# Kernel optimization log

Measured on AMD Instinct MI355X. Metric: run time of the kernel, lower is better.

Reference implementation:

```python
import jax, jax.numpy as jnp
import numpy as np

N_TOTAL = 60000   # real + ghost particles (positions/features rows)
N_REAL = 54000    # query/output particles
N_GHOST = N_TOTAL - N_REAL
N_EDGES = 1_000_000
FEAT = 32
SIZE = 3          # RBF basis functions per spatial dim -> 9 tensor-product basis


def setup_inputs() -> dict:
    key = jax.random.key(0)
    ks = jax.random.split(key, 9)
    positions = jax.random.uniform(ks[0], (N_TOTAL, 2), dtype=jnp.float32)
    output = jax.random.uniform(ks[1], (N_REAL, 2), dtype=jnp.float32)
    features = jax.random.normal(ks[2], (N_TOTAL, FEAT), dtype=jnp.float32)
    # real nodes first (-1), then ghosts pointing at a real node index
    ghostIndices = jnp.concatenate([
        jnp.full((N_REAL,), -1, dtype=jnp.int32),
        jax.random.randint(ks[3], (N_GHOST,), 0, N_REAL, dtype=jnp.int32),
    ])
    row = jax.random.randint(ks[4], (N_EDGES,), 0, N_TOTAL, dtype=jnp.int32)  # source (positions)
    col = jax.random.randint(ks[5], (N_EDGES,), 0, N_REAL, dtype=jnp.int32)   # target (output)
    edge_index = jnp.stack([row, col], axis=0)
    support = jnp.float32(0.1)
    scale = 1.0 / np.sqrt(SIZE * SIZE * FEAT)
    W0 = jax.random.normal(ks[6], (SIZE * SIZE, FEAT, FEAT), dtype=jnp.float32) * scale
    W1 = jax.random.normal(ks[7], (SIZE * SIZE, FEAT, FEAT), dtype=jnp.float32) * scale
    W2 = jax.random.normal(ks[8], (SIZE * SIZE, FEAT, FEAT), dtype=jnp.float32) * scale
    return {"positions": positions, "features": features, "output": output,
            "ghostIndices": ghostIndices, "support": support,
            "edge_index": edge_index, "W0": W0, "W1": W1, "W2": W2}


def _rbf_basis(pseudo, size=SIZE):
    """Gaussian tensor-product RBF basis over 2D pseudo-coords in [-1,1]. -> [E, size*size]"""
    centers = jnp.linspace(-1.0, 1.0, size, dtype=pseudo.dtype)
    gamma = (size - 1) / 2.0  # inverse of center spacing
    phi = jnp.exp(-(gamma * (pseudo[..., None] - centers)) ** 2)  # [E, 2, size]
    u, v = phi[:, 0, :], phi[:, 1, :]
    return (u[:, :, None] * v[:, None, :]).reshape(pseudo.shape[0], size * size)


def reference(positions, features, output, ghostIndices, support, edge_index, W0, W1, W2):
    row, col = edge_index[0], edge_index[1]
    M = output.shape[0]
    # per-edge pseudo coordinates: gather, subtract, normalize, clamp
    pseudo = jnp.clip((output[col] - positions[row]) / support, -1.0, 1.0)  # [E, 2]
    basis = _rbf_basis(pseudo)  # [E, 9]
    ghosts = ghostIndices[M:]   # layout: real nodes first, so these are the != -1 entries
    ans = features
    for W, act in ((W0, True), (W1, True), (W2, False)):
        x_src = ans[row]  # [E, k] gather source features (all nodes incl. ghosts)
        # aggregate basis-weighted features at target nodes, then one dense contraction
        T = jax.ops.segment_sum(basis[:, :, None] * x_src[:, None, :], col,
                                num_segments=M)          # [M, 9, k]
        out = jnp.einsum('mbk,bkl->ml', T, W)            # [M, l]
        if act:
            out = jax.nn.relu(out)
        ghostFeatures = out[ghosts]                      # index_select of ghost mirrors
        ans = jnp.concatenate([out, ghostFeatures], axis=0)  # [N_total, l]
    return ans
```

## Files before the change

kernel.cpp:

```cpp
#include <hip/hip_runtime.h>
#include <hip/hip_fp16.h>
#include <hip/hip_bf16.h>

#define M_REAL   54000
#define N_TOT    60000
#define N_EDGE   1000000

typedef __attribute__((ext_vector_type(8)))  short short8;
typedef __attribute__((ext_vector_type(16))) float f32x16;
typedef __attribute__((ext_vector_type(4)))  unsigned int uint4n;

__global__ void build_kernel(const int* __restrict__ row,
                             const int* __restrict__ col,
                             const int* __restrict__ ghost,
                             const float* __restrict__ positions,
                             const float* __restrict__ outpos,
                             const float* __restrict__ supportp,
                             int* __restrict__ counts,
                             uint4n* __restrict__ bucketData,
                             int maxdeg) {
    int e = blockIdx.x * blockDim.x + threadIdx.x;
    if (e >= N_EDGE) return;
    const int c = col[e];
    const int r = row[e];
    const int rm = (r < M_REAL) ? r : ghost[r];
    const float invs = 1.0f / supportp[0];
    float du = (outpos[2 * c]     - positions[2 * r])     * invs;
    float dv = (outpos[2 * c + 1] - positions[2 * r + 1]) * invs;
    du = fminf(fmaxf(du, -1.0f), 1.0f);
    dv = fminf(fmaxf(dv, -1.0f), 1.0f);
    const float u0 = __expf(-(du + 1.f) * (du + 1.f));
    const float u1 = __expf(-du * du);
    const float u2 = __expf(-(du - 1.f) * (du - 1.f));
    const float v0 = __expf(-(dv + 1.f) * (dv + 1.f));
    const float v1 = __expf(-dv * dv);
    const float v2 = __expf(-(dv - 1.f) * (dv - 1.f));
    __half2 h01 = __floats2half2_rn(u0, u1);
    __half2 h20 = __floats2half2_rn(u2, v0);
    __half2 h12 = __floats2half2_rn(v1, v2);
    uint4n d;
    d.x = (unsigned)r | ((unsigned)rm << 16);
    d.y = *reinterpret_cast<unsigned*>(&h01);
    d.z = *reinterpret_cast<unsigned*>(&h20);
    d.w = *reinterpret_cast<unsigned*>(&h12);
    int p = atomicAdd(&counts[c], 1);
    if (p < maxdeg) bucketData[(size_t)c * maxdeg + p] = d;
}

__global__ void pad_kernel(int* __restrict__ counts,
                           uint4n* __restrict__ bucketData,
                           int maxdeg) {
    int m = blockIdx.x * blockDim.x + threadIdx.x;
    if (m >= M_REAL) return;
    int deg = counts[m];
    if (deg > maxdeg) deg = maxdeg;
    int deg4 = (deg + 3) & ~3;
    uint4n z = {0u, 0u, 0u, 0u};
    for (int p = deg; p < deg4; ++p)
        bucketData[(size_t)m * maxdeg + p] = z;
    counts[m] = deg4;
}

__global__ void wprep_kernel(const float* __restrict__ W0,
                             const float* __restrict__ W1,
                             const float* __restrict__ W2,
                             unsigned short* __restrict__ Wt) {
    int i = blockIdx.x * blockDim.x + threadIdx.x;
    if (i >= 3 * 9216) return;
    const int layer = i / 9216;
    const int rem   = i % 9216;
    const int k     = rem >> 5;
    const int l     = rem & 31;
    const float* src = (layer == 0) ? W0 : (layer == 1 ? W1 : W2);
    __hip_bfloat16 b = __float2bfloat16(src[rem]);
    Wt[layer * 9216 + l * 288 + k] = __builtin_bit_cast(unsigned short, b);
}

__global__ __launch_bounds__(256) void edge_kernel(
        const float* __restrict__ xin,
        const int*   __restrict__ counts,
        const uint4n* __restrict__ bucketData,
        unsigned short* __restrict__ Tb,
        int use_hi, int maxdeg) {
    const int lane = threadIdx.x & 31;
    const int slot = threadIdx.x >> 5;
    const int m = blockIdx.x * 8 + slot;

    float t[9];
#pragma unroll
    for (int b = 0; b < 9; ++b) t[b] = 0.0f;

    const int deg4 = counts[m];
    const uint4n* bd = bucketData + (size_t)m * maxdeg;

    for (int i = 0; i < deg4; i += 4) {
        uint4n q[4];
#pragma unroll
        for (int j = 0; j < 4; ++j) q[j] = bd[i + j];
        float x[4];
#pragma unroll
        for (int j = 0; j < 4; ++j) {
            const unsigned rr = use_hi ? (q[j].x >> 16) : (q[j].x & 0xffffu);
            x[j] = xin[(size_t)rr * 32 + lane];
        }
#pragma unroll
        for (int j = 0; j < 4; ++j) {
            unsigned qy = q[j].y, qz = q[j].z, qw = q[j].w;
            const float2 U01  = __half22float2(*reinterpret_cast<const __half2*>(&qy));
            const float2 U2V0 = __half22float2(*reinterpret_cast<const __half2*>(&qz));
            const float2 V12  = __half22float2(*reinterpret_cast<const __half2*>(&qw));
            const float xv = x[j];
            const float vx0 = U2V0.y * xv;
            const float vx1 = V12.x * xv;
            const float vx2 = V12.y * xv;
            t[0] += U01.x * vx0;  t[1] += U01.x * vx1;  t[2] += U01.x * vx2;
            t[3] += U01.y * vx0;  t[4] += U01.y * vx1;  t[5] += U01.y * vx2;
            t[6] += U2V0.x * vx0; t[7] += U2V0.x * vx1; t[8] += U2V0.x * vx2;
        }
    }

    unsigned short* tr = Tb + (size_t)m * 288 + lane;
#pragma unroll
    for (int b = 0; b < 9; ++b) {
        __hip_bfloat16 h = __float2bfloat16(t[b]);
        tr[b * 32] = __builtin_bit_cast(unsigned short, h);
    }
}

__global__ __launch_bounds__(256, 2) void gemm_kernel(
        const unsigned short* __restrict__ Tb,
        const unsigned short* __restrict__ Wt,
        float* __restrict__ yout,
        int act) {
    const int wave = threadIdx.x >> 6;
    const int lane = threadIdx.x & 63;
    const int col  = lane & 31;
    const int kh   = lane >> 5;
    const int m0   = (blockIdx.x * 4 + wave) * 32;

    const int row  = m0 + col;
    const int rowc = (row < M_REAL) ? row : (M_REAL - 1);
    const uint4n* a = reinterpret_cast<const uint4n*>(Tb + (size_t)rowc * 288) + kh;
    const uint4n* b = reinterpret_cast<const uint4n*>(Wt + (size_t)col * 288) + kh;

    f32x16 acc = {};
#pragma unroll
    for (int s = 0; s < 18; ++s) {
        union { uint4n u; short8 v; } av, bv;
        av.u = a[s * 2];
        bv.u = b[s * 2];
        acc = __builtin_amdgcn_mfma_f32_32x32x16_bf16(av.v, bv.v, acc, 0, 0, 0);
    }

#pragma unroll
    for (int r = 0; r < 16; ++r) {
        const int rr = (r & 3) + 8 * (r >> 2) + 4 * kh;
        const int om = m0 + rr;
        float v = acc[r];
        if (act) v = fmaxf(v, 0.0f);
        if (om < M_REAL) yout[om * 32 + col] = v;
    }
}

__global__ void ghost_kernel(const int* __restrict__ ghost,
                             float* __restrict__ out) {
    int idx = blockIdx.x * blockDim.x + threadIdx.x;
    if (idx >= (N_TOT - M_REAL) * 32) return;
    int i = idx >> 5;
    int k = idx & 31;
    int g = ghost[M_REAL + i];
    out[(M_REAL + i) * 32 + k] = out[g * 32 + k];
}

extern "C" void kernel_launch(void* const* d_in, const int* in_sizes, int n_in,
                              void* d_out, int out_size, void* d_ws, size_t ws_size,
                              hipStream_t stream) {
    const float* positions = (const float*)d_in[0];
    const float* features  = (const float*)d_in[1];
    const float* outpos    = (const float*)d_in[2];
    const int*   ghost     = (const int*)d_in[3];
    const float* support   = (const float*)d_in[4];
    const int*   edge      = (const int*)d_in[5];
    const float* W0        = (const float*)d_in[6];
    const float* W1        = (const float*)d_in[7];
    const float* W2        = (const float*)d_in[8];
    float* out = (float*)d_out;

    auto al = [](size_t x) { return (x + 255) & ~(size_t)255; };
    const size_t countsB = al((size_t)M_REAL * 4);
    const size_t TbB     = al((size_t)M_REAL * 288 * 2);
    const size_t WtB     = al((size_t)3 * 9216 * 2);
    const size_t outB    = al((size_t)M_REAL * 32 * 4);
    const size_t need64  = countsB + (size_t)M_REAL * 64 * 16 + TbB + WtB + outB;
    const int maxdeg = (ws_size >= need64) ? 64 : 48;

    char* ws = (char*)d_ws;
    int*            counts     = (int*)ws;            ws += countsB;
    uint4n*         bucketData = (uint4n*)ws;         ws += (size_t)M_REAL * maxdeg * 16;
    unsigned short* Tb         = (unsigned short*)ws; ws += TbB;
    unsigned short* Wt         = (unsigned short*)ws; ws += WtB;
    float*          out1       = (float*)ws;
    float*          out0       = out;

    const int* erow = edge;
    const int* ecol = edge + N_EDGE;

    (void)hipMemsetAsync(counts, 0, (size_t)M_REAL * 4, stream);
    build_kernel<<<(N_EDGE + 255) / 256, 256, 0, stream>>>(
        erow, ecol, ghost, positions, outpos, support, counts, bucketData, maxdeg);
    pad_kernel<<<(M_REAL + 255) / 256, 256, 0, stream>>>(counts, bucketData, maxdeg);
    wprep_kernel<<<(3 * 9216 + 255) / 256, 256, 0, stream>>>(W0, W1, W2, Wt);

    const int egrid = M_REAL / 8;
    const int ggrid = 422;

    edge_kernel<<<egrid, 256, 0, stream>>>(features, counts, bucketData, Tb, 0, maxdeg);
    gemm_kernel<<<ggrid, 256, 0, stream>>>(Tb, Wt, out0, 1);
    edge_kernel<<<egrid, 256, 0, stream>>>(out0, counts, bucketData, Tb, 1, maxdeg);
    gemm_kernel<<<ggrid, 256, 0, stream>>>(Tb, Wt + 9216, out1, 1);
    edge_kernel<<<egrid, 256, 0, stream>>>(out1, counts, bucketData, Tb, 1, maxdeg);
    gemm_kernel<<<ggrid, 256, 0, stream>>>(Tb, Wt + 2 * 9216, out, 0);

    ghost_kernel<<<((N_TOT - M_REAL) * 32 + 255) / 256, 256, 0, stream>>>(ghost, out);
}
```

Measured before the change: 194.5 us.

## Replace fixed-capacity per-node buckets with compact CSR via count, scan, scatter

Edge binning moves from fixed maxdeg-slot buckets per target node, padded to multiples of 4, to a compact CSR layout built with a count pass, a single-block prefix scan and an atomic-cursor scatter. The edge kernel now reads by offsets and masks tail entries instead of relying on zero padding. This removes the silent truncation of edges above maxdeg, and the compact layout may improve cache locality of the edge stream. In exchange it adds an extra pass over col and a serial single-block scan, and edge reads are no longer 4-aligned per node.

```diff
diff --git a/kernel.cpp b/kernel.cpp
--- a/kernel.cpp
+++ b/kernel.cpp
@@ -10,15 +10,54 @@
 typedef __attribute__((ext_vector_type(16))) float f32x16;
 typedef __attribute__((ext_vector_type(4)))  unsigned int uint4n;
 
-__global__ void build_kernel(const int* __restrict__ row,
-                             const int* __restrict__ col,
-                             const int* __restrict__ ghost,
-                             const float* __restrict__ positions,
-                             const float* __restrict__ outpos,
-                             const float* __restrict__ supportp,
-                             int* __restrict__ counts,
-                             uint4n* __restrict__ bucketData,
-                             int maxdeg) {
+__global__ void count_kernel(const int* __restrict__ col,
+                             int* __restrict__ counts) {
+    int e = blockIdx.x * blockDim.x + threadIdx.x;
+    if (e >= N_EDGE) return;
+    atomicAdd(&counts[col[e]], 1);
+}
+
+__global__ __launch_bounds__(256) void scan_kernel(
+        const int* __restrict__ counts,
+        int* __restrict__ offsets,
+        int* __restrict__ cursor,
+        uint4n* __restrict__ bucketData) {
+    __shared__ int part[256];
+    const int tid = threadIdx.x;
+    const int CH = (M_REAL + 255) / 256;
+    const int lo = tid * CH;
+    const int hi = (lo + CH < M_REAL) ? lo + CH : M_REAL;
+    int s = 0;
+    for (int i = lo; i < hi; ++i) s += counts[i];
+    part[tid] = s;
+    __syncthreads();
+    for (int d = 1; d < 256; d <<= 1) {
+        int t = (tid >= d) ? part[tid - d] : 0;
+        __syncthreads();
+        if (tid >= d) part[tid] += t;
+        __syncthreads();
+    }
+    int run = part[tid] - s;
+    for (int i = lo; i < hi; ++i) {
+        offsets[i] = run;
+        cursor[i]  = run;
+        run += counts[i];
+    }
+    if (tid == 255) offsets[M_REAL] = part[255];
+    if (tid < 4) {
+        uint4n z = {0u, 0u, 0u, 0u};
+        bucketData[N_EDGE + tid] = z;
+    }
+}
+
+__global__ void scatter_kernel(const int* __restrict__ row,
+                               const int* __restrict__ col,
+                               const int* __restrict__ ghost,
+                               const float* __restrict__ positions,
+                               const float* __restrict__ outpos,
+                               const float* __restrict__ supportp,
+                               int* __restrict__ cursor,
+                               uint4n* __restrict__ bucketData) {
     int e = blockIdx.x * blockDim.x + threadIdx.x;
     if (e >= N_EDGE) return;
     const int c = col[e];
@@ -43,22 +82,8 @@
     d.y = *reinterpret_cast<unsigned*>(&h01);
     d.z = *reinterpret_cast<unsigned*>(&h20);
     d.w = *reinterpret_cast<unsigned*>(&h12);
-    int p = atomicAdd(&counts[c], 1);
-    if (p < maxdeg) bucketData[(size_t)c * maxdeg + p] = d;
-}
-
-__global__ void pad_kernel(int* __restrict__ counts,
-                           uint4n* __restrict__ bucketData,
-                           int maxdeg) {
-    int m = blockIdx.x * blockDim.x + threadIdx.x;
-    if (m >= M_REAL) return;
-    int deg = counts[m];
-    if (deg > maxdeg) deg = maxdeg;
-    int deg4 = (deg + 3) & ~3;
-    uint4n z = {0u, 0u, 0u, 0u};
-    for (int p = deg; p < deg4; ++p)
-        bucketData[(size_t)m * maxdeg + p] = z;
-    counts[m] = deg4;
+    int p = atomicAdd(&cursor[c], 1);
+    bucketData[p] = d;
 }
 
 __global__ void wprep_kernel(const float* __restrict__ W0,
@@ -78,10 +103,10 @@
 
 __global__ __launch_bounds__(256) void edge_kernel(
         const float* __restrict__ xin,
-        const int*   __restrict__ counts,
+        const int*   __restrict__ offsets,
         const uint4n* __restrict__ bucketData,
         unsigned short* __restrict__ Tb,
-        int use_hi, int maxdeg) {
+        int use_hi) {
     const int lane = threadIdx.x & 31;
     const int slot = threadIdx.x >> 5;
     const int m = blockIdx.x * 8 + slot;
@@ -90,10 +115,11 @@
 #pragma unroll
     for (int b = 0; b < 9; ++b) t[b] = 0.0f;
 
-    const int deg4 = counts[m];
-    const uint4n* bd = bucketData + (size_t)m * maxdeg;
-
-    for (int i = 0; i < deg4; i += 4) {
+    const int beg = offsets[m];
+    const int deg = offsets[m + 1] - beg;
+    const uint4n* bd = bucketData + beg;
+
+    for (int i = 0; i < deg; i += 4) {
         uint4n q[4];
 #pragma unroll
         for (int j = 0; j < 4; ++j) q[j] = bd[i + j];
@@ -101,7 +127,8 @@
 #pragma unroll
         for (int j = 0; j < 4; ++j) {
             const unsigned rr = use_hi ? (q[j].x >> 16) : (q[j].x & 0xffffu);
-            x[j] = xin[(size_t)rr * 32 + lane];
+            const float xv = xin[(size_t)rr * 32 + lane];
+            x[j] = (i + j < deg) ? xv : 0.0f;
         }
 #pragma unroll
         for (int j = 0; j < 4; ++j) {
@@ -187,18 +214,13 @@
     float* out = (float*)d_out;
 
     auto al = [](size_t x) { return (x + 255) & ~(size_t)255; };
-    const size_t countsB = al((size_t)M_REAL * 4);
-    const size_t TbB     = al((size_t)M_REAL * 288 * 2);
-    const size_t WtB     = al((size_t)3 * 9216 * 2);
-    const size_t outB    = al((size_t)M_REAL * 32 * 4);
-    const size_t need64  = countsB + (size_t)M_REAL * 64 * 16 + TbB + WtB + outB;
-    const int maxdeg = (ws_size >= need64) ? 64 : 48;
-
     char* ws = (char*)d_ws;
-    int*            counts     = (int*)ws;            ws += countsB;
-    uint4n*         bucketData = (uint4n*)ws;         ws += (size_t)M_REAL * maxdeg * 16;
-    unsigned short* Tb         = (unsigned short*)ws; ws += TbB;
-    unsigned short* Wt         = (unsigned short*)ws; ws += WtB;
+    int*            counts     = (int*)ws;            ws += al((size_t)M_REAL * 4);
+    int*            offsets    = (int*)ws;            ws += al((size_t)(M_REAL + 1) * 4);
+    int*            cursor     = (int*)ws;            ws += al((size_t)M_REAL * 4);
+    uint4n*         bucketData = (uint4n*)ws;         ws += al((size_t)(N_EDGE + 4) * 16);
+    unsigned short* Tb         = (unsigned short*)ws; ws += al((size_t)M_REAL * 288 * 2);
+    unsigned short* Wt         = (unsigned short*)ws; ws += al((size_t)3 * 9216 * 2);
     float*          out1       = (float*)ws;
     float*          out0       = out;
 
@@ -206,19 +228,20 @@
     const int* ecol = edge + N_EDGE;
 
     (void)hipMemsetAsync(counts, 0, (size_t)M_REAL * 4, stream);
-    build_kernel<<<(N_EDGE + 255) / 256, 256, 0, stream>>>(
-        erow, ecol, ghost, positions, outpos, support, counts, bucketData, maxdeg);
-    pad_kernel<<<(M_REAL + 255) / 256, 256, 0, stream>>>(counts, bucketData, maxdeg);
+    count_kernel<<<(N_EDGE + 255) / 256, 256, 0, stream>>>(ecol, counts);
+    scan_kernel<<<1, 256, 0, stream>>>(counts, offsets, cursor, bucketData);
+    scatter_kernel<<<(N_EDGE + 255) / 256, 256, 0, stream>>>(
+        erow, ecol, ghost, positions, outpos, support, cursor, bucketData);
     wprep_kernel<<<(3 * 9216 + 255) / 256, 256, 0, stream>>>(W0, W1, W2, Wt);
 
     const int egrid = M_REAL / 8;
     const int ggrid = 422;
 
-    edge_kernel<<<egrid, 256, 0, stream>>>(features, counts, bucketData, Tb, 0, maxdeg);
+    edge_kernel<<<egrid, 256, 0, stream>>>(features, offsets, bucketData, Tb, 0);
     gemm_kernel<<<ggrid, 256, 0, stream>>>(Tb, Wt, out0, 1);
-    edge_kernel<<<egrid, 256, 0, stream>>>(out0, counts, bucketData, Tb, 1, maxdeg);
+    edge_kernel<<<egrid, 256, 0, stream>>>(out0, offsets, bucketData, Tb, 1);
     gemm_kernel<<<ggrid, 256, 0, stream>>>(Tb, Wt + 9216, out1, 1);
-    edge_kernel<<<egrid, 256, 0, stream>>>(out1, counts, bucketData, Tb, 1, maxdeg);
+    edge_kernel<<<egrid, 256, 0, stream>>>(out1, offsets, bucketData, Tb, 1);
     gemm_kernel<<<ggrid, 256, 0, stream>>>(Tb, Wt + 2 * 9216, out, 0);
 
     ghost_kernel<<<((N_TOT - M_REAL) * 32 + 255) / 256, 256, 0, stream>>>(ghost, out);
```

Measured after the change: 351.5 us. 1.81x slower.

## Fuse edge aggregation and MFMA contraction into one per-layer kernel via LDS

Applied to the files above, without the earlier changes.

Merges the per-layer edge aggregation and the bf16 MFMA GEMM into a single kernel. Each block aggregates 32 target nodes into a padded shared-memory tile, then one wave runs the 32x32x288 contraction from LDS. This removes the global round trip of the T buffer and three kernel launches. In exchange, only one wave out of four does the GEMM, each block serialises four nodes per half-wave, and the __syncthreads barrier can leave lanes idle when degrees are uneven.

```diff
diff --git a/kernel.cpp b/kernel.cpp
--- a/kernel.cpp
+++ b/kernel.cpp
@@ -5,6 +5,7 @@
 #define M_REAL   54000
 #define N_TOT    60000
 #define N_EDGE   1000000
+#define TSTRIDE  296
 
 typedef __attribute__((ext_vector_type(8)))  short short8;
 typedef __attribute__((ext_vector_type(16))) float f32x16;
@@ -76,89 +77,87 @@
     Wt[layer * 9216 + l * 288 + k] = __builtin_bit_cast(unsigned short, b);
 }
 
-__global__ __launch_bounds__(256) void edge_kernel(
+__global__ __launch_bounds__(256) void conv_kernel(
         const float* __restrict__ xin,
         const int*   __restrict__ counts,
         const uint4n* __restrict__ bucketData,
-        unsigned short* __restrict__ Tb,
-        int use_hi, int maxdeg) {
-    const int lane = threadIdx.x & 31;
-    const int slot = threadIdx.x >> 5;
-    const int m = blockIdx.x * 8 + slot;
-
-    float t[9];
-#pragma unroll
-    for (int b = 0; b < 9; ++b) t[b] = 0.0f;
-
-    const int deg4 = counts[m];
-    const uint4n* bd = bucketData + (size_t)m * maxdeg;
-
-    for (int i = 0; i < deg4; i += 4) {
-        uint4n q[4];
-#pragma unroll
-        for (int j = 0; j < 4; ++j) q[j] = bd[i + j];
-        float x[4];
-#pragma unroll
-        for (int j = 0; j < 4; ++j) {
-            const unsigned rr = use_hi ? (q[j].x >> 16) : (q[j].x & 0xffffu);
-            x[j] = xin[(size_t)rr * 32 + lane];
-        }
-#pragma unroll
-        for (int j = 0; j < 4; ++j) {
-            unsigned qy = q[j].y, qz = q[j].z, qw = q[j].w;
-            const float2 U01  = __half22float2(*reinterpret_cast<const __half2*>(&qy));
-            const float2 U2V0 = __half22float2(*reinterpret_cast<const __half2*>(&qz));
-            const float2 V12  = __half22float2(*reinterpret_cast<const __half2*>(&qw));
-            const float xv = x[j];
-            const float vx0 = U2V0.y * xv;
-            const float vx1 = V12.x * xv;
-            const float vx2 = V12.y * xv;
-            t[0] += U01.x * vx0;  t[1] += U01.x * vx1;  t[2] += U01.x * vx2;
-            t[3] += U01.y * vx0;  t[4] += U01.y * vx1;  t[5] += U01.y * vx2;
-            t[6] += U2V0.x * vx0; t[7] += U2V0.x * vx1; t[8] += U2V0.x * vx2;
-        }
-    }
-
-    unsigned short* tr = Tb + (size_t)m * 288 + lane;
-#pragma unroll
-    for (int b = 0; b < 9; ++b) {
-        __hip_bfloat16 h = __float2bfloat16(t[b]);
-        tr[b * 32] = __builtin_bit_cast(unsigned short, h);
-    }
-}
-
-__global__ __launch_bounds__(256, 2) void gemm_kernel(
-        const unsigned short* __restrict__ Tb,
         const unsigned short* __restrict__ Wt,
         float* __restrict__ yout,
-        int act) {
-    const int wave = threadIdx.x >> 6;
-    const int lane = threadIdx.x & 63;
-    const int col  = lane & 31;
-    const int kh   = lane >> 5;
-    const int m0   = (blockIdx.x * 4 + wave) * 32;
-
-    const int row  = m0 + col;
-    const int rowc = (row < M_REAL) ? row : (M_REAL - 1);
-    const uint4n* a = reinterpret_cast<const uint4n*>(Tb + (size_t)rowc * 288) + kh;
-    const uint4n* b = reinterpret_cast<const uint4n*>(Wt + (size_t)col * 288) + kh;
-
-    f32x16 acc = {};
-#pragma unroll
-    for (int s = 0; s < 18; ++s) {
-        union { uint4n u; short8 v; } av, bv;
-        av.u = a[s * 2];
-        bv.u = b[s * 2];
-        acc = __builtin_amdgcn_mfma_f32_32x32x16_bf16(av.v, bv.v, acc, 0, 0, 0);
+        int act, int use_hi, int maxdeg) {
+    __shared__ unsigned short Tl[32 * TSTRIDE];
+
+    const int lane = threadIdx.x & 31;
+    const int hw   = threadIdx.x >> 5;
+    const int m0   = blockIdx.x * 32;
+
+    for (int r = 0; r < 4; ++r) {
+        const int dl = hw * 4 + r;
+        const int m  = m0 + dl;
+
+        float t[9];
+#pragma unroll
+        for (int b = 0; b < 9; ++b) t[b] = 0.0f;
+
+        if (m < M_REAL) {
+            const int deg4 = counts[m];
+            const uint4n* bd = bucketData + (size_t)m * maxdeg;
+            for (int i = 0; i < deg4; i += 4) {
+                uint4n q[4];
+#pragma unroll
+                for (int j = 0; j < 4; ++j) q[j] = bd[i + j];
+                float x[4];
+#pragma unroll
+                for (int j = 0; j < 4; ++j) {
+                    const unsigned rr = use_hi ? (q[j].x >> 16) : (q[j].x & 0xffffu);
+                    x[j] = xin[(size_t)rr * 32 + lane];
+                }
+#pragma unroll
+                for (int j = 0; j < 4; ++j) {
+                    unsigned qy = q[j].y, qz = q[j].z, qw = q[j].w;
+                    const float2 U01  = __half22float2(*reinterpret_cast<const __half2*>(&qy));
+                    const float2 U2V0 = __half22float2(*reinterpret_cast<const __half2*>(&qz));
+                    const float2 V12  = __half22float2(*reinterpret_cast<const __half2*>(&qw));
+                    const float xv = x[j];
+                    const float vx0 = U2V0.y * xv;
+                    const float vx1 = V12.x * xv;
+                    const float vx2 = V12.y * xv;
+                    t[0] += U01.x * vx0;  t[1] += U01.x * vx1;  t[2] += U01.x * vx2;
+                    t[3] += U01.y * vx0;  t[4] += U01.y * vx1;  t[5] += U01.y * vx2;
+                    t[6] += U2V0.x * vx0; t[7] += U2V0.x * vx1; t[8] += U2V0.x * vx2;
+                }
+            }
+        }
+        unsigned short* tr = &Tl[dl * TSTRIDE + lane];
+#pragma unroll
+        for (int b = 0; b < 9; ++b) {
+            __hip_bfloat16 h = __float2bfloat16(t[b]);
+            tr[b * 32] = __builtin_bit_cast(unsigned short, h);
+        }
     }
-
-#pragma unroll
-    for (int r = 0; r < 16; ++r) {
-        const int rr = (r & 3) + 8 * (r >> 2) + 4 * kh;
-        const int om = m0 + rr;
-        float v = acc[r];
-        if (act) v = fmaxf(v, 0.0f);
-        if (om < M_REAL) yout[om * 32 + col] = v;
+    __syncthreads();
+
+    if (threadIdx.x < 64) {
+        const int l31 = threadIdx.x & 31;
+        const int kh  = threadIdx.x >> 5;
+        const unsigned short* brow = Wt + (size_t)l31 * 288 + kh * 8;
+
+        f32x16 acc = {};
+#pragma unroll
+        for (int s = 0; s < 18; ++s) {
+            short8 av = *reinterpret_cast<const short8*>(&Tl[l31 * TSTRIDE + s * 16 + kh * 8]);
+            union { uint4n u; short8 v; } bv;
+            bv.u = *reinterpret_cast<const uint4n*>(brow + s * 16);
+            acc = __builtin_amdgcn_mfma_f32_32x32x16_bf16(av, bv.v, acc, 0, 0, 0);
+        }
+
+#pragma unroll
+        for (int r = 0; r < 16; ++r) {
+            const int rr = (r & 3) + 8 * (r >> 2) + 4 * kh;
+            const int om = m0 + rr;
+            float v = acc[r];
+            if (act) v = fmaxf(v, 0.0f);
+            if (om < M_REAL) yout[om * 32 + l31] = v;
+        }
     }
 }
 
@@ -188,16 +187,14 @@
 
     auto al = [](size_t x) { return (x + 255) & ~(size_t)255; };
     const size_t countsB = al((size_t)M_REAL * 4);
-    const size_t TbB     = al((size_t)M_REAL * 288 * 2);
     const size_t WtB     = al((size_t)3 * 9216 * 2);
     const size_t outB    = al((size_t)M_REAL * 32 * 4);
-    const size_t need64  = countsB + (size_t)M_REAL * 64 * 16 + TbB + WtB + outB;
+    const size_t need64  = countsB + (size_t)M_REAL * 64 * 16 + WtB + outB;
     const int maxdeg = (ws_size >= need64) ? 64 : 48;
 
     char* ws = (char*)d_ws;
     int*            counts     = (int*)ws;            ws += countsB;
     uint4n*         bucketData = (uint4n*)ws;         ws += (size_t)M_REAL * maxdeg * 16;
-    unsigned short* Tb         = (unsigned short*)ws; ws += TbB;
     unsigned short* Wt         = (unsigned short*)ws; ws += WtB;
     float*          out1       = (float*)ws;
     float*          out0       = out;
@@ -211,15 +208,14 @@
     pad_kernel<<<(M_REAL + 255) / 256, 256, 0, stream>>>(counts, bucketData, maxdeg);
     wprep_kernel<<<(3 * 9216 + 255) / 256, 256, 0, stream>>>(W0, W1, W2, Wt);
 
-    const int egrid = M_REAL / 8;
-    const int ggrid = 422;
-
-    edge_kernel<<<egrid, 256, 0, stream>>>(features, counts, bucketData, Tb, 0, maxdeg);
-    gemm_kernel<<<ggrid, 256, 0, stream>>>(Tb, Wt, out0, 1);
-    edge_kernel<<<egrid, 256, 0, stream>>>(out0, counts, bucketData, Tb, 1, maxdeg);
-    gemm_kernel<<<ggrid, 256, 0, stream>>>(Tb, Wt + 9216, out1, 1);
-    edge_kernel<<<egrid, 256, 0, stream>>>(out1, counts, bucketData, Tb, 1, maxdeg);
-    gemm_kernel<<<ggrid, 256, 0, stream>>>(Tb, Wt + 2 * 9216, out, 0);
+    const int cgrid = (M_REAL + 31) / 32;
+
+    conv_kernel<<<cgrid, 256, 0, stream>>>(features, counts, bucketData, Wt,
+                                           out0, 1, 0, maxdeg);
+    conv_kernel<<<cgrid, 256, 0, stream>>>(out0, counts, bucketData, Wt + 9216,
+                                           out1, 1, 1, maxdeg);
+    conv_kernel<<<cgrid, 256, 0, stream>>>(out1, counts, bucketData, Wt + 2 * 9216,
+                                           out, 0, 1, maxdeg);
 
     ghost_kernel<<<((N_TOT - M_REAL) * 32 + 255) / 256, 256, 0, stream>>>(ghost, out);
 }
```

Measured after the change: 204.0 us. 1.05x slower.
